# Optimization experiments

Hardware: AMD Instinct MI355X
Metric: run time of the kernel (lower is better)

## Reference

```python
import jax, jax.numpy as jnp
import numpy as np

N, E, G, D, L = 10000, 160000, 100, 128, 5
LMAX, SHD, VOCAB = 2, 9, 10
S3 = 3.0 ** 0.5


def _sph(v):
    # e3nn spherical harmonics, normalize=True, normalization='norm' (||Y_l||=1), lmax=2
    r = jnp.linalg.norm(v, axis=-1, keepdims=True)
    u = v / jnp.maximum(r, 1e-12)
    x, y, z = u[:, 0], u[:, 1], u[:, 2]
    y2 = jnp.stack([S3 * x * z, S3 * x * y, y * y - 0.5 * (x * x + z * z), S3 * y * z, 0.5 * S3 * (z * z - x * x)], axis=-1)
    return jnp.concatenate([jnp.ones_like(u[:, :1]), u, y2], axis=-1)  # [E,9]


def _sh_scale(s, w):
    # FullyConnectedTensorProduct(sh, 1x0e, sh): per-l scaling by weight w [.,3]
    return jnp.concatenate([s[:, 0:1] * w[:, 0:1], s[:, 1:4] * w[:, 1:2], s[:, 4:9] * w[:, 2:3]], axis=-1)


def _smean(src, idx, n):
    s = jax.ops.segment_sum(src, idx, num_segments=n)
    c = jax.ops.segment_sum(jnp.ones((src.shape[0], 1), src.dtype), idx, num_segments=n)
    return s / jnp.maximum(c, 1.0)


def _mlp(x, w1, b1, w2, b2, last_act=False):
    h = jax.nn.silu(x @ w1 + b1)
    o = h @ w2 + b2
    return jax.nn.silu(o) if last_act else o


def _forward(atoms, edge_index, batch_ids, pos, emb_table, Wsi1, bsi1, Wsi2, bsi2, WsiC1, bsiC1, WsiC2, bsiC2, Wm1, bm1, Wm2, bm2, Wp1, bp1, Wp2, bp2, Wn1, bn1, Wn2, bn2, Ws1, bs1, Ws2, bs2, Wpred, bpred):
    row, col = edge_index[0], edge_index[1]
    feat = emb_table[atoms]                                  # [N,D]
    # --- SH_INIT ---
    dpos = pos[row] - pos[col]
    dist = jnp.linalg.norm(dpos, axis=-1, keepdims=True)
    msg = _mlp(jnp.concatenate([dist, feat[row], feat[col]], axis=-1), Wsi1, bsi1, Wsi2, bsi2)
    dsh = _sh_scale(jax.lax.stop_gradient(_sph(dpos)), msg)
    sh = _smean(dsh, row, N)                                 # [N,9]
    pos_com = _smean(pos, batch_ids, G)[batch_ids]
    sh = sh + _sh_scale(jax.lax.stop_gradient(_sph(pos - pos_com)), _mlp(feat, WsiC1, bsiC1, WsiC2, bsiC2))
    sh = sh.at[:, :LMAX * LMAX].set(0.0)                     # all_ell=False: keep only highest l
    # --- stacked HEGNN layers via scan ---
    def body(carry, p):
        feat, pos, sh = carry
        wm1, cm1, wm2, cm2, wp1, cp1, wp2, cp2, wn1, cn1, wn2, cn2, ws1, cs1, ws2, cs2 = p
        dp = pos[row] - pos[col]
        d2 = jnp.sum(dp * dp, axis=-1, keepdims=True)        # squared distance
        t = sh[row] * sh[col]
        ip = jnp.concatenate([jnp.sum(t[:, 0:1], -1, keepdims=True), jnp.sum(t[:, 1:4], -1, keepdims=True), jnp.sum(t[:, 4:9], -1, keepdims=True)], axis=-1)
        m = _mlp(jnp.concatenate([feat[row], feat[col], d2, ip], axis=-1), wm1, cm1, wm2, cm2, last_act=True)
        dp = dp * _mlp(m, wp1, cp1, wp2, cp2)
        ds = _sh_scale(sh[row] - sh[col], _mlp(m, ws1, cs1, ws2, cs2))
        m_agg = _smean(m, row, N)
        p_agg = _smean(dp, row, N)
        s_agg = _smean(ds, row, N)
        sh = sh + s_agg
        pos = pos + p_agg
        feat = _mlp(jnp.concatenate([feat, m_agg], axis=-1), wn1, cn1, wn2, cn2)
        return (feat, pos, sh), None
    (feat, pos, sh), _ = jax.lax.scan(body, (feat, pos, sh), (Wm1, bm1, Wm2, bm2, Wp1, bp1, Wp2, bp2, Wn1, bn1, Wn2, bn2, Ws1, bs1, Ws2, bs2))
    # --- equivariant sum-pool + linear pred ---
    pooled = jax.ops.segment_sum(jnp.concatenate([feat, pos, sh], axis=-1), batch_ids, num_segments=G)
    return pooled @ Wpred + bpred                            # [G,1]


def setup_inputs():
    ks = iter(jax.random.split(jax.random.key(0), 48))
    def nrm(shape):
        return jax.random.normal(next(ks), shape, jnp.float32)
    def w(shape):
        return nrm(shape) / np.float32(np.sqrt(shape[-2]))
    z = lambda *s: jnp.zeros(s, jnp.float32)
    inp = dict(
        atoms=jax.random.randint(next(ks), (N,), 0, VOCAB),
        edge_index=jax.random.randint(next(ks), (2, E), 0, N),
        batch_ids=jnp.sort(jax.random.randint(next(ks), (N,), 0, G)),
        pos=nrm((N, 3)),
        emb_table=nrm((VOCAB, D)) * 0.1,
    )
    inp.update(Wsi1=w((2 * D + 1, D)), bsi1=z(D), Wsi2=w((D, LMAX + 1)), bsi2=z(LMAX + 1),
               WsiC1=w((D, D)), bsiC1=z(D), WsiC2=w((D, LMAX + 1)), bsiC2=z(LMAX + 1))
    inp.update(Wm1=w((L, 2 * D + 1 + LMAX + 1, D)), bm1=z(L, D), Wm2=w((L, D, D)), bm2=z(L, D),
               Wp1=w((L, D, D)), bp1=z(L, D), Wp2=w((L, D, 1)), bp2=z(L, 1),
               Wn1=w((L, 2 * D, D)), bn1=z(L, D), Wn2=w((L, D, D)), bn2=z(L, D),
               Ws1=w((L, D, D)), bs1=z(L, D), Ws2=w((L, D, LMAX + 1)), bs2=z(L, LMAX + 1),
               Wpred=w((D + 3 + SHD, 1)), bpred=z(1))
    return inp


def reference(atoms, edge_index, batch_ids, pos, emb_table, Wsi1, bsi1, Wsi2, bsi2, WsiC1, bsiC1, WsiC2, bsiC2, Wm1, bm1, Wm2, bm2, Wp1, bp1, Wp2, bp2, Wn1, bn1, Wn2, bn2, Ws1, bs1, Ws2, bs2, Wpred, bpred):
    return _forward(atoms, edge_index, batch_ids, pos, emb_table, Wsi1, bsi1, Wsi2, bsi2, WsiC1, bsiC1, WsiC2, bsiC2, Wm1, bm1, Wm2, bm2, Wp1, bp1, Wp2, bp2, Wn1, bn1, Wn2, bn2, Ws1, bs1, Ws2, bs2, Wpred, bpred)
```

## Files before the change

### kernel.cpp

```cpp
#include <hip/hip_runtime.h>
#include <math.h>

#define NA 10000
#define NE 160000
#define NG 100
#define DF 128
#define NL 5
#define NAP 10112
#define NSB 40

typedef __attribute__((ext_vector_type(8))) short bfx8;
typedef __attribute__((ext_vector_type(4))) float f32x4;

__device__ __forceinline__ float silu_f(float x) {
    return x / (1.0f + __expf(-x));
}

__device__ __forceinline__ unsigned short f2bf(float x) {
    unsigned u = __builtin_bit_cast(unsigned, x);
    u = (u + 0x7FFFu + ((u >> 16) & 1u)) >> 16;
    return (unsigned short)u;
}
__device__ __forceinline__ float bf2f(unsigned short h) {
    unsigned u = ((unsigned)h) << 16;
    return __builtin_bit_cast(float, u);
}
__device__ __forceinline__ unsigned packbf(float lo, float hi) {
    return (unsigned)f2bf(lo) | ((unsigned)f2bf(hi) << 16);
}

__device__ __forceinline__ void sph9(float dx, float dy, float dz, float* s) {
    float r = sqrtf(dx * dx + dy * dy + dz * dz);
    float inv = 1.0f / fmaxf(r, 1e-12f);
    float x = dx * inv, y = dy * inv, z = dz * inv;
    const float S3 = 1.7320508075688772f;
    s[0] = 1.0f;
    s[1] = x; s[2] = y; s[3] = z;
    s[4] = S3 * x * z;
    s[5] = S3 * x * y;
    s[6] = y * y - 0.5f * (x * x + z * z);
    s[7] = S3 * y * z;
    s[8] = 0.5f * S3 * (z * z - x * x);
}

#define OFF_SI1   0
#define OFF_SIC1  36864
#define LBASE     53248
#define LSIZE     135168
#define LOFF_M1   0
#define LOFF_M2   36864
#define LOFF_P1   53248
#define LOFF_S1   69632
#define LOFF_N1   86016
#define LOFF_N2   118784
#define WT_TOTAL  729088

__global__ void k_prep_w(const float* __restrict__ Wsi1, const float* __restrict__ WsiC1,
                         const float* __restrict__ Wm1, const float* __restrict__ Wm2,
                         const float* __restrict__ Wp1, const float* __restrict__ Ws1,
                         const float* __restrict__ Wn1, const float* __restrict__ Wn2,
                         unsigned short* __restrict__ WT) {
    int flat = blockIdx.x * 256 + threadIdx.x;
    if (flat >= WT_TOTAL) return;
    float v = 0.0f;
    if (flat < OFF_SIC1) {
        int o = flat - OFF_SI1;
        int n = o / 288, k = o % 288;
        if (k < 256)       v = Wsi1[(k + 1) * 128 + n];
        else if (k == 256) v = Wsi1[n];
    } else if (flat < LBASE) {
        int o = flat - OFF_SIC1;
        int n = o / 128, k = o % 128;
        v = WsiC1[k * 128 + n];
    } else {
        int t = flat - LBASE;
        int lyr = t / LSIZE;
        int o = t % LSIZE;
        if (o < LOFF_M2) {
            int n = o / 288, k = o % 288;
            if (k < 260) v = Wm1[(size_t)lyr * 260 * 128 + k * 128 + n];
        } else if (o < LOFF_P1) {
            int o2 = o - LOFF_M2; int n = o2 / 128, k = o2 % 128;
            v = Wm2[(size_t)lyr * 16384 + k * 128 + n];
        } else if (o < LOFF_S1) {
            int o2 = o - LOFF_P1; int n = o2 / 128, k = o2 % 128;
            v = Wp1[(size_t)lyr * 16384 + k * 128 + n];
        } else if (o < LOFF_N1) {
            int o2 = o - LOFF_S1; int n = o2 / 128, k = o2 % 128;
            v = Ws1[(size_t)lyr * 16384 + k * 128 + n];
        } else if (o < LOFF_N2) {
            int o2 = o - LOFF_N1; int n = o2 / 256, k = o2 % 256;
            v = Wn1[(size_t)lyr * 32768 + k * 128 + n];
        } else {
            int o2 = o - LOFF_N2; int n = o2 / 128, k = o2 % 128;
            v = Wn2[(size_t)lyr * 16384 + k * 128 + n];
        }
    }
    WT[flat] = f2bf(v);
}

template <int KP, int MODE, bool ACT, int NOUT, bool F32OUT>
__global__ __launch_bounds__(256) void gemm_mfma(
    const unsigned short* __restrict__ Ab,
    const unsigned short* __restrict__ WT,
    const float* __restrict__ bias, int M,
    const int* __restrict__ rowI, const int* __restrict__ colI,
    const unsigned short* __restrict__ featb, const unsigned short* __restrict__ tailb,
    unsigned short* __restrict__ Cb, float* __restrict__ Cf,
    const float* __restrict__ W2, const float* __restrict__ b2,
    float* __restrict__ outS)
{
    constexpr int NO = (NOUT > 0) ? NOUT : 1;
    __shared__ unsigned short As[128 * 40];
    __shared__ unsigned short Bs[128 * 40];
    __shared__ float W2s[NOUT > 0 ? 128 * NO : 1];
    __shared__ float red[NOUT > 0 ? 128 * 8 * NO : 1];

    const int tid = threadIdx.x;
    const int m0 = blockIdx.x * 128;
    const int mlo = tid >> 2;
    const int part = tid & 3;

    if (NOUT > 0) {
        for (int t = tid; t < 128 * NO; t += 256) W2s[t] = W2[t];
    }

    int er0 = 0, ec0 = 0, er1 = 0, ec1 = 0;
    if (MODE == 1) {
        er0 = rowI[m0 + mlo];      ec0 = colI[m0 + mlo];
        er1 = rowI[m0 + mlo + 64]; ec1 = colI[m0 + mlo + 64];
    }

    const int w = tid >> 6;
    const int l = tid & 63;
    const int quad = l >> 4;
    const int lm = l & 15;
    const int wm = (w >> 1) * 64, wn = (w & 1) * 64;

    float bv[4];
#pragma unroll
    for (int j = 0; j < 4; j++) bv[j] = bias[wn + j * 16 + lm];

    f32x4 acc[4][4] = {};

    constexpr int NCH = KP / 32;
#pragma unroll 1
    for (int c = 0; c < NCH; c++) {
        const int k0 = c * 32;
#pragma unroll
        for (int i = 0; i < 2; i++) {
            const int m = mlo + i * 64;
            uint4 v;
            if (MODE == 0) {
                v = *(const uint4*)(Ab + (size_t)(m0 + m) * KP + k0 + part * 8);
            } else {
                if (k0 < 128) {
                    int e = i ? er1 : er0;
                    v = *(const uint4*)(featb + (size_t)e * 128 + k0 + part * 8);
                } else if (k0 < 256) {
                    int e = i ? ec1 : ec0;
                    v = *(const uint4*)(featb + (size_t)e * 128 + (k0 - 128) + part * 8);
                } else {
                    if (part == 0) v = *(const uint4*)(tailb + (size_t)(m0 + m) * 16);
                    else           v = make_uint4(0, 0, 0, 0);
                }
            }
            *(uint4*)&As[m * 40 + part * 8] = v;
            uint4 wv = *(const uint4*)(WT + (size_t)m * KP + k0 + part * 8);
            *(uint4*)&Bs[m * 40 + part * 8] = wv;
        }
        __syncthreads();
        bfx8 a[4], b[4];
#pragma unroll
        for (int i = 0; i < 4; i++) a[i] = *(const bfx8*)&As[(wm + i * 16 + lm) * 40 + quad * 8];
#pragma unroll
        for (int j = 0; j < 4; j++) b[j] = *(const bfx8*)&Bs[(wn + j * 16 + lm) * 40 + quad * 8];
#pragma unroll
        for (int i = 0; i < 4; i++)
#pragma unroll
            for (int j = 0; j < 4; j++)
                acc[i][j] = __builtin_amdgcn_mfma_f32_16x16x32_bf16(a[i], b[j], acc[i][j], 0, 0, 0);
        __syncthreads();
    }

    if (NOUT > 0) {
        const int slot = (w & 1) * 4 + (lm >> 2);
#pragma unroll
        for (int i = 0; i < 4; i++) {
#pragma unroll
            for (int r = 0; r < 4; r++) {
                const int rowL = wm + i * 16 + quad * 4 + r;
                float ps[NO];
#pragma unroll
                for (int o = 0; o < NO; o++) ps[o] = 0.0f;
#pragma unroll
                for (int j = 0; j < 4; j++) {
                    float v = silu_f(acc[i][j][r] + bv[j]);
                    const int colg = wn + j * 16 + lm;
#pragma unroll
                    for (int o = 0; o < NO; o++) ps[o] += v * W2s[colg * NO + o];
                }
#pragma unroll
                for (int off = 1; off <= 2; off <<= 1)
#pragma unroll
                    for (int o = 0; o < NO; o++) ps[o] += __shfl_xor(ps[o], off, 64);
                if ((lm & 3) == 0)
#pragma unroll
                    for (int o = 0; o < NO; o++)
                        red[(rowL * 8 + slot) * NO + o] = ps[o];
            }
        }
        __syncthreads();
        for (int t = tid; t < 128 * NO; t += 256) {
            int rowL = t / NO, o = t - rowL * NO;
            float s = 0.0f;
#pragma unroll
            for (int k = 0; k < 8; k++) s += red[(rowL * 8 + k) * NO + o];
            int e = m0 + rowL;
            if (e < M) outS[(size_t)e * NO + o] = s + b2[o];
        }
    } else {
#pragma unroll
        for (int i = 0; i < 4; i++) {
            const int rbase = wm + i * 16 + quad * 4;
#pragma unroll
            for (int r = 0; r < 4; r++) {
                const int e = m0 + rbase + r;
                if (e >= M) continue;
#pragma unroll
                for (int j = 0; j < 4; j++) {
                    float v = acc[i][j][r] + bv[j];
                    if (ACT) v = silu_f(v);
                    const int colg = wn + j * 16 + lm;
                    Cb[(size_t)e * 128 + colg] = f2bf(v);
                    if (F32OUT) Cf[(size_t)e * 128 + colg] = v;
                }
            }
        }
    }
}

__global__ void k_count_edges(const int* __restrict__ row, int* __restrict__ cnt) {
    int e = blockIdx.x * blockDim.x + threadIdx.x;
    if (e < NE) atomicAdd(&cnt[row[e]], 1);
}

__global__ void k_scan_block(const int* __restrict__ cnt, int* __restrict__ ptr,
                             int* __restrict__ btot) {
    __shared__ int s[256];
    int tid = threadIdx.x;
    int i = blockIdx.x * 256 + tid;
    int v = (i < NA) ? cnt[i] : 0;
    s[tid] = v;
    __syncthreads();
    for (int off = 1; off < 256; off <<= 1) {
        int t = (tid >= off) ? s[tid - off] : 0;
        __syncthreads();
        s[tid] += t;
        __syncthreads();
    }
    if (i < NA) ptr[i] = s[tid] - v;
    if (tid == 255) btot[blockIdx.x] = s[255];
}

__global__ void k_scan_tot(int* __restrict__ btot) {
    int lane = threadIdx.x;
    int v = (lane < NSB) ? btot[lane] : 0;
    int orig = v;
    for (int off = 1; off < 64; off <<= 1) {
        int t = __shfl_up(v, off, 64);
        if (lane >= off) v += t;
    }
    if (lane < NSB) btot[lane] = v - orig;
}

__global__ void k_scan_add(int* __restrict__ ptr, const int* __restrict__ btot) {
    int i = blockIdx.x * 256 + threadIdx.x;
    if (i < NA) ptr[i] += btot[i >> 8];
    if (i == 0) ptr[NA] = NE;
}

__global__ void k_copy_cursor(const int* __restrict__ ptr, int* __restrict__ cursor) {
    int i = blockIdx.x * 256 + threadIdx.x;
    if (i < NA) cursor[i] = ptr[i];
}

__global__ void k_sort(const int* __restrict__ row, const int* __restrict__ col,
                       int* __restrict__ cursor,
                       int* __restrict__ row_s, int* __restrict__ col_s) {
    int e = blockIdx.x * blockDim.x + threadIdx.x;
    if (e >= NE) return;
    int r = row[e];
    int p = atomicAdd(&cursor[r], 1);
    row_s[p] = r;
    col_s[p] = col[e];
}

__global__ void k_gptr(const int* __restrict__ bid, int* __restrict__ gptr) {
    int n = blockIdx.x * blockDim.x + threadIdx.x;
    if (n >= NA) return;
    int b = bid[n];
    int bp = (n == 0) ? -1 : bid[n - 1];
    for (int g = bp + 1; g <= b; g++) gptr[g] = n;
    if (n == NA - 1)
        for (int g = b + 1; g <= NG; g++) gptr[g] = NA;
}

__global__ void k_init_feat(const int* __restrict__ atoms,
                            const float* __restrict__ emb,
                            float* __restrict__ feat, unsigned short* __restrict__ featb) {
    int idx = blockIdx.x * blockDim.x + threadIdx.x;
    if (idx >= NA * DF) return;
    float v = emb[atoms[idx >> 7] * DF + (idx & 127)];
    feat[idx] = v;
    featb[idx] = f2bf(v);
}

__global__ void k_copy_pos(const float* __restrict__ pos, float* __restrict__ posc) {
    int idx = blockIdx.x * blockDim.x + threadIdx.x;
    if (idx < NA * 3) posc[idx] = pos[idx];
}

__global__ void k_com_g(const float* __restrict__ pos, const int* __restrict__ gptr,
                        float* __restrict__ com) {
    int g = blockIdx.x;
    int lane = threadIdx.x;
    int s0 = gptr[g], s1 = gptr[g + 1];
    float sx = 0.0f, sy = 0.0f, sz = 0.0f;
    for (int n = s0 + lane; n < s1; n += 64) {
        sx += pos[n * 3 + 0];
        sy += pos[n * 3 + 1];
        sz += pos[n * 3 + 2];
    }
#pragma unroll
    for (int off = 32; off > 0; off >>= 1) {
        sx += __shfl_down(sx, off, 64);
        sy += __shfl_down(sy, off, 64);
        sz += __shfl_down(sz, off, 64);
    }
    if (lane == 0) {
        float cinv = 1.0f / fmaxf((float)(s1 - s0), 1.0f);
        com[g * 3 + 0] = sx * cinv;
        com[g * 3 + 1] = sy * cinv;
        com[g * 3 + 2] = sz * cinv;
    }
}

__global__ void k_tail_init(const int* __restrict__ row, const int* __restrict__ col,
                            const float* __restrict__ pos, unsigned short* __restrict__ tailb) {
    int e = blockIdx.x * blockDim.x + threadIdx.x;
    if (e >= NE) return;
    int r = row[e], c = col[e];
    float dx = pos[r * 3 + 0] - pos[c * 3 + 0];
    float dy = pos[r * 3 + 1] - pos[c * 3 + 1];
    float dz = pos[r * 3 + 2] - pos[c * 3 + 2];
    float dist = sqrtf(dx * dx + dy * dy + dz * dz);
    uint4 t0 = make_uint4(packbf(dist, 0.0f), 0, 0, 0);
    uint4 z = make_uint4(0, 0, 0, 0);
    *(uint4*)(tailb + (size_t)e * 16) = t0;
    *(uint4*)(tailb + (size_t)e * 16 + 8) = z;
}

__global__ void k_edge_pre(const int* __restrict__ row, const int* __restrict__ col,
                           const float* __restrict__ pos, const float* __restrict__ sh,
                           unsigned short* __restrict__ tailb) {
    int e = blockIdx.x * blockDim.x + threadIdx.x;
    if (e >= NE) return;
    int r = row[e], c = col[e];
    float dx = pos[r * 3 + 0] - pos[c * 3 + 0];
    float dy = pos[r * 3 + 1] - pos[c * 3 + 1];
    float dz = pos[r * 3 + 2] - pos[c * 3 + 2];
    float d2 = dx * dx + dy * dy + dz * dz;
    const float* sr = sh + (size_t)r * 9;
    const float* sc = sh + (size_t)c * 9;
    float ip0 = sr[0] * sc[0];
    float ip1 = sr[1] * sc[1] + sr[2] * sc[2] + sr[3] * sc[3];
    float ip2 = sr[4] * sc[4] + sr[5] * sc[5] + sr[6] * sc[6] + sr[7] * sc[7] + sr[8] * sc[8];
    uint4 t0 = make_uint4(packbf(d2, ip0), packbf(ip1, ip2), 0, 0);
    uint4 z = make_uint4(0, 0, 0, 0);
    *(uint4*)(tailb + (size_t)e * 16) = t0;
    *(uint4*)(tailb + (size_t)e * 16 + 8) = z;
}

__global__ void k_gather_sph(const int* __restrict__ ptr, const int* __restrict__ col_s,
                             const float* __restrict__ pos, const float* __restrict__ msg,
                             float* __restrict__ sh_mean) {
    int n = blockIdx.x;
    int lane = threadIdx.x;
    int s0 = ptr[n], s1 = ptr[n + 1];
    float px = pos[n * 3 + 0], py = pos[n * 3 + 1], pz = pos[n * 3 + 2];
    float a[9];
#pragma unroll
    for (int j = 0; j < 9; j++) a[j] = 0.0f;
    for (int e = s0 + lane; e < s1; e += 64) {
        int c = col_s[e];
        float dx = px - pos[c * 3 + 0];
        float dy = py - pos[c * 3 + 1];
        float dz = pz - pos[c * 3 + 2];
        float s[9];
        sph9(dx, dy, dz, s);
        float w0 = msg[e * 3 + 0], w1 = msg[e * 3 + 1], w2 = msg[e * 3 + 2];
        a[0] += s[0] * w0;
        a[1] += s[1] * w1; a[2] += s[2] * w1; a[3] += s[3] * w1;
        a[4] += s[4] * w2; a[5] += s[5] * w2; a[6] += s[6] * w2;
        a[7] += s[7] * w2; a[8] += s[8] * w2;
    }
#pragma unroll
    for (int off = 32; off > 0; off >>= 1)
#pragma unroll
        for (int j = 0; j < 9; j++) a[j] += __shfl_down(a[j], off, 64);
    if (lane == 0) {
        float cinv = 1.0f / fmaxf((float)(s1 - s0), 1.0f);
#pragma unroll
        for (int j = 0; j < 9; j++) sh_mean[(size_t)n * 9 + j] = a[j] * cinv;
    }
}

__global__ void k_sh_finish(const float* __restrict__ sh_mean,
                            const float* __restrict__ pos, const float* __restrict__ com,
                            const int* __restrict__ bid, const float* __restrict__ msgC,
                            float* __restrict__ sh) {
    int n = blockIdx.x * blockDim.x + threadIdx.x;
    if (n >= NA) return;
    int b = bid[n];
    float dx = pos[n * 3 + 0] - com[b * 3 + 0];
    float dy = pos[n * 3 + 1] - com[b * 3 + 1];
    float dz = pos[n * 3 + 2] - com[b * 3 + 2];
    float s[9];
    sph9(dx, dy, dz, s);
    float w2 = msgC[n * 3 + 2];
    sh[n * 9 + 0] = 0.0f;
    sh[n * 9 + 1] = 0.0f;
    sh[n * 9 + 2] = 0.0f;
    sh[n * 9 + 3] = 0.0f;
#pragma unroll
    for (int j = 4; j < 9; j++)
        sh[n * 9 + j] = sh_mean[(size_t)n * 9 + j] + s[j] * w2;
}

__global__ void k_gather_ps_upd(const int* __restrict__ ptr, const int* __restrict__ col_s,
                                const float* __restrict__ pos, const float* __restrict__ sh,
                                const float* __restrict__ psc, const float* __restrict__ ssc,
                                float* __restrict__ pos_new, float* __restrict__ sh_new) {
    int n = blockIdx.x;
    int lane = threadIdx.x;
    int s0 = ptr[n], s1 = ptr[n + 1];
    float px = pos[n * 3 + 0], py = pos[n * 3 + 1], pz = pos[n * 3 + 2];
    float shn[9];
#pragma unroll
    for (int j = 0; j < 9; j++) shn[j] = sh[(size_t)n * 9 + j];
    float a[12];
#pragma unroll
    for (int j = 0; j < 12; j++) a[j] = 0.0f;
    for (int e = s0 + lane; e < s1; e += 64) {
        int c = col_s[e];
        float p = psc[e];
        a[0] += (px - pos[c * 3 + 0]) * p;
        a[1] += (py - pos[c * 3 + 1]) * p;
        a[2] += (pz - pos[c * 3 + 2]) * p;
        float w0 = ssc[e * 3 + 0], w1 = ssc[e * 3 + 1], w2 = ssc[e * 3 + 2];
        const float* sc = sh + (size_t)c * 9;
        a[3]  += (shn[0] - sc[0]) * w0;
        a[4]  += (shn[1] - sc[1]) * w1;
        a[5]  += (shn[2] - sc[2]) * w1;
        a[6]  += (shn[3] - sc[3]) * w1;
        a[7]  += (shn[4] - sc[4]) * w2;
        a[8]  += (shn[5] - sc[5]) * w2;
        a[9]  += (shn[6] - sc[6]) * w2;
        a[10] += (shn[7] - sc[7]) * w2;
        a[11] += (shn[8] - sc[8]) * w2;
    }
#pragma unroll
    for (int off = 32; off > 0; off >>= 1)
#pragma unroll
        for (int j = 0; j < 12; j++) a[j] += __shfl_down(a[j], off, 64);
    if (lane == 0) {
        float cinv = 1.0f / fmaxf((float)(s1 - s0), 1.0f);
        pos_new[n * 3 + 0] = px + a[0] * cinv;
        pos_new[n * 3 + 1] = py + a[1] * cinv;
        pos_new[n * 3 + 2] = pz + a[2] * cinv;
#pragma unroll
        for (int j = 0; j < 9; j++) sh_new[(size_t)n * 9 + j] = shn[j] + a[3 + j] * cinv;
    }
}

__global__ __launch_bounds__(128) void k_gather_xn(
    const int* __restrict__ ptr, const unsigned short* __restrict__ bufMb,
    const unsigned short* __restrict__ featb, unsigned short* __restrict__ Xnb) {
    int n = blockIdx.x;
    int c = threadIdx.x;
    int s0 = ptr[n], s1 = ptr[n + 1];
    float sum = 0.0f;
    for (int e = s0; e < s1; e++) sum += bf2f(bufMb[(size_t)e * 128 + c]);
    float cinv = 1.0f / fmaxf((float)(s1 - s0), 1.0f);
    Xnb[(size_t)n * 256 + c] = featb[(size_t)n * 128 + c];
    Xnb[(size_t)n * 256 + 128 + c] = f2bf(sum * cinv);
}

__global__ __launch_bounds__(192) void k_pool_pred(
    const int* __restrict__ gptr, const float* __restrict__ feat,
    const float* __restrict__ pos, const float* __restrict__ sh,
    const float* __restrict__ Wp, const float* __restrict__ bp,
    float* __restrict__ out) {
    __shared__ float pl[140];
    int g = blockIdx.x;
    int c = threadIdx.x;
    int s0 = gptr[g], s1 = gptr[g + 1];
    if (c < 140) {
        float sum = 0.0f;
        for (int n = s0; n < s1; n++) {
            float v;
            if (c < 128)      v = feat[(size_t)n * 128 + c];
            else if (c < 131) v = pos[n * 3 + (c - 128)];
            else              v = sh[(size_t)n * 9 + (c - 131)];
            sum += v;
        }
        pl[c] = sum;
    }
    __syncthreads();
    if (c < 64) {
        float s = 0.0f;
        for (int k = c; k < 140; k += 64) s += pl[k] * Wp[k];
#pragma unroll
        for (int off = 32; off > 0; off >>= 1) s += __shfl_down(s, off, 64);
        if (c == 0) out[g] = s + bp[0];
    }
}

extern "C" void kernel_launch(void* const* d_in, const int* in_sizes, int n_in,
                              void* d_out, int out_size, void* d_ws, size_t ws_size,
                              hipStream_t stream) {
    const int*   atoms  = (const int*)d_in[0];
    const int*   eidx   = (const int*)d_in[1];
    const int*   row    = eidx;
    const int*   col    = eidx + NE;
    const int*   bid    = (const int*)d_in[2];
    const float* pos_in = (const float*)d_in[3];
    const float* emb    = (const float*)d_in[4];
    const float* Wsi1   = (const float*)d_in[5];
    const float* bsi1   = (const float*)d_in[6];
    const float* Wsi2   = (const float*)d_in[7];
    const float* bsi2   = (const float*)d_in[8];
    const float* WsiC1  = (const float*)d_in[9];
    const float* bsiC1  = (const float*)d_in[10];
    const float* WsiC2  = (const float*)d_in[11];
    const float* bsiC2  = (const float*)d_in[12];
    const float* Wm1    = (const float*)d_in[13];
    const float* bm1    = (const float*)d_in[14];
    const float* Wm2    = (const float*)d_in[15];
    const float* bm2    = (const float*)d_in[16];
    const float* Wp1    = (const float*)d_in[17];
    const float* bp1    = (const float*)d_in[18];
    const float* Wp2    = (const float*)d_in[19];
    const float* bp2    = (const float*)d_in[20];
    const float* Wn1    = (const float*)d_in[21];
    const float* bn1    = (const float*)d_in[22];
    const float* Wn2    = (const float*)d_in[23];
    const float* bn2    = (const float*)d_in[24];
    const float* Ws1    = (const float*)d_in[25];
    const float* bs1    = (const float*)d_in[26];
    const float* Ws2    = (const float*)d_in[27];
    const float* bs2    = (const float*)d_in[28];
    const float* Wpred  = (const float*)d_in[29];
    const float* bpred  = (const float*)d_in[30];

    float* base = (float*)d_ws;
    size_t off = 0;
    auto alloc = [&](size_t nfl) { float* r = base + off; off += nfl; return r; };
    unsigned short* bufHb = (unsigned short*)alloc((size_t)NE * DF / 2);
    unsigned short* bufMb = (unsigned short*)alloc((size_t)NE * DF / 2);
    unsigned short* featb = (unsigned short*)alloc((size_t)NAP * DF / 2);
    unsigned short* hnb   = (unsigned short*)alloc((size_t)NAP * DF / 2);
    unsigned short* Xnb   = (unsigned short*)alloc((size_t)NAP * 256 / 2);
    unsigned short* tailb = (unsigned short*)alloc((size_t)NE * 16 / 2);
    unsigned short* WT    = (unsigned short*)alloc(WT_TOTAL / 2);
    float* feat    = alloc((size_t)NAP * DF);
    float* sc3     = alloc((size_t)NE * 3);
    float* psc     = alloc(NE);
    float* pos0    = alloc((size_t)NA * 3 + 4);
    float* pos1    = alloc((size_t)NA * 3 + 4);
    float* sh0     = alloc((size_t)NA * 9 + 4);
    float* sh1     = alloc((size_t)NA * 9 + 4);
    float* sh_mean = alloc((size_t)NA * 9 + 4);
    float* com     = alloc(NG * 3 + 4);
    float* msgC    = alloc((size_t)NA * 3 + 4);
    int* cnt_row   = (int*)alloc(NA);
    int* ptr       = (int*)alloc(NA + 4);
    int* cursor    = (int*)alloc(NA);
    int* gptr      = (int*)alloc(NG + 4);
    int* row_s     = (int*)alloc(NE);
    int* col_s     = (int*)alloc(NE);
    int* btot      = (int*)alloc(64);

    const dim3 B256(256);
    const int gE = NE / 128;
    const int gN = NAP / 128;

    hipMemsetAsync(cnt_row, 0, NA * sizeof(int), stream);
    k_prep_w<<<(WT_TOTAL + 255) / 256, B256, 0, stream>>>(Wsi1, WsiC1, Wm1, Wm2, Wp1, Ws1, Wn1, Wn2, WT);
    k_init_feat<<<(NA * DF + 255) / 256, B256, 0, stream>>>(atoms, emb, feat, featb);
    k_copy_pos<<<(NA * 3 + 255) / 256, B256, 0, stream>>>(pos_in, pos0);
    k_count_edges<<<(NE + 255) / 256, B256, 0, stream>>>(row, cnt_row);
    k_scan_block<<<NSB, B256, 0, stream>>>(cnt_row, ptr, btot);
    k_scan_tot<<<1, 64, 0, stream>>>(btot);
    k_scan_add<<<NSB, B256, 0, stream>>>(ptr, btot);
    k_copy_cursor<<<NSB, B256, 0, stream>>>(ptr, cursor);
    k_sort<<<(NE + 255) / 256, B256, 0, stream>>>(row, col, cursor, row_s, col_s);
    k_gptr<<<(NA + 255) / 256, B256, 0, stream>>>(bid, gptr);
    k_com_g<<<NG, 64, 0, stream>>>(pos_in, gptr, com);

    k_tail_init<<<(NE + 255) / 256, B256, 0, stream>>>(row_s, col_s, pos0, tailb);
    gemm_mfma<288, 1, true, 3, false><<<gE, B256, 0, stream>>>(
        nullptr, WT + OFF_SI1, bsi1, NE, row_s, col_s, featb, tailb,
        nullptr, nullptr, Wsi2, bsi2, sc3);
    k_gather_sph<<<NA, 64, 0, stream>>>(ptr, col_s, pos0, sc3, sh_mean);
    gemm_mfma<128, 0, true, 3, false><<<gN, B256, 0, stream>>>(
        featb, WT + OFF_SIC1, bsiC1, NA, nullptr, nullptr, nullptr, nullptr,
        nullptr, nullptr, WsiC2, bsiC2, msgC);
    k_sh_finish<<<(NA + 255) / 256, B256, 0, stream>>>(sh_mean, pos0, com, bid, msgC, sh0);

    float* posA = pos0; float* posB = pos1;
    float* shA = sh0;   float* shB = sh1;

    for (int l = 0; l < NL; l++) {
        const unsigned short* wtL = WT + LBASE + (size_t)l * LSIZE;
        const float* cm1 = bm1 + l * 128;
        const float* cm2 = bm2 + l * 128;
        const float* cp1 = bp1 + l * 128;
        const float* wp2 = Wp2 + (size_t)l * 128;
        const float* cp2 = bp2 + l;
        const float* cn1 = bn1 + l * 128;
        const float* cn2 = bn2 + l * 128;
        const float* cs1 = bs1 + l * 128;
        const float* ws2 = Ws2 + (size_t)l * 128 * 3;
        const float* cs2 = bs2 + l * 3;

        k_edge_pre<<<(NE + 255) / 256, B256, 0, stream>>>(row_s, col_s, posA, shA, tailb);
        gemm_mfma<288, 1, true, 0, false><<<gE, B256, 0, stream>>>(
            nullptr, wtL + LOFF_M1, cm1, NE, row_s, col_s, featb, tailb,
            bufHb, nullptr, nullptr, nullptr, nullptr);
        gemm_mfma<128, 0, true, 0, false><<<gE, B256, 0, stream>>>(
            bufHb, wtL + LOFF_M2, cm2, NE, nullptr, nullptr, nullptr, nullptr,
            bufMb, nullptr, nullptr, nullptr, nullptr);
        gemm_mfma<128, 0, true, 1, false><<<gE, B256, 0, stream>>>(
            bufMb, wtL + LOFF_P1, cp1, NE, nullptr, nullptr, nullptr, nullptr,
            nullptr, nullptr, wp2, cp2, psc);
        gemm_mfma<128, 0, true, 3, false><<<gE, B256, 0, stream>>>(
            bufMb, wtL + LOFF_S1, cs1, NE, nullptr, nullptr, nullptr, nullptr,
            nullptr, nullptr, ws2, cs2, sc3);
        k_gather_ps_upd<<<NA, 64, 0, stream>>>(ptr, col_s, posA, shA, psc, sc3, posB, shB);
        k_gather_xn<<<NA, 128, 0, stream>>>(ptr, bufMb, featb, Xnb);
        gemm_mfma<256, 0, true, 0, false><<<gN, B256, 0, stream>>>(
            Xnb, wtL + LOFF_N1, cn1, NA, nullptr, nullptr, nullptr, nullptr,
            hnb, nullptr, nullptr, nullptr, nullptr);
        gemm_mfma<128, 0, false, 0, true><<<gN, B256, 0, stream>>>(
            hnb, wtL + LOFF_N2, cn2, NA, nullptr, nullptr, nullptr, nullptr,
            featb, feat, nullptr, nullptr, nullptr);

        float* tp = posA; posA = posB; posB = tp;
        float* ts = shA;  shA = shB;  shB = ts;
    }

    k_pool_pred<<<NG, 192, 0, stream>>>(gptr, feat, posA, shA, Wpred, bpred, (float*)d_out);
}
```

Before: 1.046 ms.

## Factor edge first-layer GEMM into per-node projections plus edge gather-add

The first edge MLP layer on concat(feat[row], feat[col], scalars) is split algebraically. feat@W_row and feat@W_col are computed once per node (10k rows) with a new dual GEMM. Each edge then gathers the two projected rows, adds the scalar-tail terms and bias in fp32, and applies SiLU, which removes a K=288 GEMM over 160k edges in the init and every layer. The position/SH gather kernel is also merged with the feature-mean gather to save a launch. The per-node projections are rounded to bf16 before summation, which slightly changes numerics.

```diff
diff --git a/kernel.cpp b/kernel.cpp
--- a/kernel.cpp
+++ b/kernel.cpp
@@ -43,17 +43,17 @@
     s[8] = 0.5f * S3 * (z * z - x * x);
 }
 
-#define OFF_SI1   0
-#define OFF_SIC1  36864
-#define LBASE     53248
-#define LSIZE     135168
-#define LOFF_M1   0
-#define LOFF_M2   36864
-#define LOFF_P1   53248
-#define LOFF_S1   69632
-#define LOFF_N1   86016
-#define LOFF_N2   118784
-#define WT_TOTAL  729088
+#define OFF_SIRC  0
+#define OFF_SICTR 32768
+#define LBASE     49152
+#define LOFF_MRC  0
+#define LOFF_M2   32768
+#define LOFF_P1   49152
+#define LOFF_S1   65536
+#define LOFF_N1   81920
+#define LOFF_N2   114688
+#define LSIZE     131072
+#define WT_TOTAL  704512
 
 __global__ void k_prep_w(const float* __restrict__ Wsi1, const float* __restrict__ WsiC1,
                          const float* __restrict__ Wm1, const float* __restrict__ Wm2,
@@ -63,49 +63,105 @@
     int flat = blockIdx.x * 256 + threadIdx.x;
     if (flat >= WT_TOTAL) return;
     float v = 0.0f;
-    if (flat < OFF_SIC1) {
-        int o = flat - OFF_SI1;
-        int n = o / 288, k = o % 288;
-        if (k < 256)       v = Wsi1[(k + 1) * 128 + n];
-        else if (k == 256) v = Wsi1[n];
+    if (flat < OFF_SICTR) {
+        int half = flat >> 14;
+        int o = flat & 16383;
+        int n = o >> 7, k = o & 127;
+        v = Wsi1[(k + 1 + half * 128) * 128 + n];
     } else if (flat < LBASE) {
-        int o = flat - OFF_SIC1;
-        int n = o / 128, k = o % 128;
+        int o = flat - OFF_SICTR;
+        int n = o >> 7, k = o & 127;
         v = WsiC1[k * 128 + n];
     } else {
         int t = flat - LBASE;
         int lyr = t / LSIZE;
         int o = t % LSIZE;
         if (o < LOFF_M2) {
-            int n = o / 288, k = o % 288;
-            if (k < 260) v = Wm1[(size_t)lyr * 260 * 128 + k * 128 + n];
+            int half = o >> 14;
+            int o2 = o & 16383;
+            int n = o2 >> 7, k = o2 & 127;
+            v = Wm1[(size_t)lyr * 33280 + (k + half * 128) * 128 + n];
         } else if (o < LOFF_P1) {
-            int o2 = o - LOFF_M2; int n = o2 / 128, k = o2 % 128;
+            int o2 = o - LOFF_M2; int n = o2 >> 7, k = o2 & 127;
             v = Wm2[(size_t)lyr * 16384 + k * 128 + n];
         } else if (o < LOFF_S1) {
-            int o2 = o - LOFF_P1; int n = o2 / 128, k = o2 % 128;
+            int o2 = o - LOFF_P1; int n = o2 >> 7, k = o2 & 127;
             v = Wp1[(size_t)lyr * 16384 + k * 128 + n];
         } else if (o < LOFF_N1) {
-            int o2 = o - LOFF_S1; int n = o2 / 128, k = o2 % 128;
+            int o2 = o - LOFF_S1; int n = o2 >> 7, k = o2 & 127;
             v = Ws1[(size_t)lyr * 16384 + k * 128 + n];
         } else if (o < LOFF_N2) {
-            int o2 = o - LOFF_N1; int n = o2 / 256, k = o2 % 256;
+            int o2 = o - LOFF_N1; int n = o2 >> 8, k = o2 & 255;
             v = Wn1[(size_t)lyr * 32768 + k * 128 + n];
         } else {
-            int o2 = o - LOFF_N2; int n = o2 / 128, k = o2 % 128;
+            int o2 = o - LOFF_N2; int n = o2 >> 7, k = o2 & 127;
             v = Wn2[(size_t)lyr * 16384 + k * 128 + n];
         }
     }
     WT[flat] = f2bf(v);
 }
 
-template <int KP, int MODE, bool ACT, int NOUT, bool F32OUT>
+__global__ __launch_bounds__(256) void k_fgemm(
+    const unsigned short* __restrict__ Ab,
+    const unsigned short* __restrict__ WT2,
+    unsigned short* __restrict__ F12)
+{
+    __shared__ unsigned short As[128 * 40];
+    __shared__ unsigned short Bs[128 * 40];
+    const unsigned short* WTp = WT2 + (size_t)blockIdx.y * 16384;
+    unsigned short* Cb = F12 + (size_t)blockIdx.y * NAP * 128;
+
+    const int tid = threadIdx.x;
+    const int m0 = blockIdx.x * 128;
+    const int mlo = tid >> 2;
+    const int part = tid & 3;
+    const int w = tid >> 6, l = tid & 63;
+    const int quad = l >> 4, lm = l & 15;
+    const int wm = (w >> 1) * 64, wn = (w & 1) * 64;
+
+    f32x4 acc[4][4] = {};
+#pragma unroll 1
+    for (int c = 0; c < 4; c++) {
+        const int k0 = c * 32;
+#pragma unroll
+        for (int i = 0; i < 2; i++) {
+            const int m = mlo + i * 64;
+            *(uint4*)&As[m * 40 + part * 8] =
+                *(const uint4*)(Ab + (size_t)(m0 + m) * 128 + k0 + part * 8);
+            *(uint4*)&Bs[m * 40 + part * 8] =
+                *(const uint4*)(WTp + (size_t)m * 128 + k0 + part * 8);
+        }
+        __syncthreads();
+        bfx8 a[4], b[4];
+#pragma unroll
+        for (int i = 0; i < 4; i++) a[i] = *(const bfx8*)&As[(wm + i * 16 + lm) * 40 + quad * 8];
+#pragma unroll
+        for (int j = 0; j < 4; j++) b[j] = *(const bfx8*)&Bs[(wn + j * 16 + lm) * 40 + quad * 8];
+#pragma unroll
+        for (int i = 0; i < 4; i++)
+#pragma unroll
+            for (int j = 0; j < 4; j++)
+                acc[i][j] = __builtin_amdgcn_mfma_f32_16x16x32_bf16(a[i], b[j], acc[i][j], 0, 0, 0);
+        __syncthreads();
+    }
+#pragma unroll
+    for (int i = 0; i < 4; i++) {
+        const int rbase = wm + i * 16 + quad * 4;
+#pragma unroll
+        for (int r = 0; r < 4; r++) {
+            const int e = m0 + rbase + r;
+#pragma unroll
+            for (int j = 0; j < 4; j++)
+                Cb[(size_t)e * 128 + wn + j * 16 + lm] = f2bf(acc[i][j][r]);
+        }
+    }
+}
+
+template <int KP, bool ACT, int NOUT, bool F32OUT>
 __global__ __launch_bounds__(256) void gemm_mfma(
     const unsigned short* __restrict__ Ab,
     const unsigned short* __restrict__ WT,
     const float* __restrict__ bias, int M,
-    const int* __restrict__ rowI, const int* __restrict__ colI,
-    const unsigned short* __restrict__ featb, const unsigned short* __restrict__ tailb,
     unsigned short* __restrict__ Cb, float* __restrict__ Cf,
     const float* __restrict__ W2, const float* __restrict__ b2,
     float* __restrict__ outS)
@@ -125,16 +181,8 @@
         for (int t = tid; t < 128 * NO; t += 256) W2s[t] = W2[t];
     }
 
-    int er0 = 0, ec0 = 0, er1 = 0, ec1 = 0;
-    if (MODE == 1) {
-        er0 = rowI[m0 + mlo];      ec0 = colI[m0 + mlo];
-        er1 = rowI[m0 + mlo + 64]; ec1 = colI[m0 + mlo + 64];
-    }
-
-    const int w = tid >> 6;
-    const int l = tid & 63;
-    const int quad = l >> 4;
-    const int lm = l & 15;
+    const int w = tid >> 6, l = tid & 63;
+    const int quad = l >> 4, lm = l & 15;
     const int wm = (w >> 1) * 64, wn = (w & 1) * 64;
 
     float bv[4];
@@ -142,7 +190,6 @@
     for (int j = 0; j < 4; j++) bv[j] = bias[wn + j * 16 + lm];
 
     f32x4 acc[4][4] = {};
-
     constexpr int NCH = KP / 32;
 #pragma unroll 1
     for (int c = 0; c < NCH; c++) {
@@ -150,24 +197,10 @@
 #pragma unroll
         for (int i = 0; i < 2; i++) {
             const int m = mlo + i * 64;
-            uint4 v;
-            if (MODE == 0) {
-                v = *(const uint4*)(Ab + (size_t)(m0 + m) * KP + k0 + part * 8);
-            } else {
-                if (k0 < 128) {
-                    int e = i ? er1 : er0;
-                    v = *(const uint4*)(featb + (size_t)e * 128 + k0 + part * 8);
-                } else if (k0 < 256) {
-                    int e = i ? ec1 : ec0;
-                    v = *(const uint4*)(featb + (size_t)e * 128 + (k0 - 128) + part * 8);
-                } else {
-                    if (part == 0) v = *(const uint4*)(tailb + (size_t)(m0 + m) * 16);
-                    else           v = make_uint4(0, 0, 0, 0);
-                }
-            }
-            *(uint4*)&As[m * 40 + part * 8] = v;
-            uint4 wv = *(const uint4*)(WT + (size_t)m * KP + k0 + part * 8);
-            *(uint4*)&Bs[m * 40 + part * 8] = wv;
+            *(uint4*)&As[m * 40 + part * 8] =
+                *(const uint4*)(Ab + (size_t)(m0 + m) * KP + k0 + part * 8);
+            *(uint4*)&Bs[m * 40 + part * 8] =
+                *(const uint4*)(WT + (size_t)m * KP + k0 + part * 8);
         }
         __syncthreads();
         bfx8 a[4], b[4];
@@ -237,6 +270,120 @@
                 }
             }
         }
+    }
+}
+
+__global__ __launch_bounds__(256) void k_edge_h(
+    const int* __restrict__ rowI, const int* __restrict__ colI,
+    const unsigned short* __restrict__ F12,
+    const float* __restrict__ pos, const float* __restrict__ sh,
+    const float* __restrict__ wtail,
+    const float* __restrict__ b1,
+    unsigned short* __restrict__ bufHb)
+{
+    __shared__ float Wt[4][128];
+    __shared__ float B1[128];
+    int tid = threadIdx.x;
+    if (tid < 128) B1[tid] = b1[tid];
+    for (int t = tid; t < 512; t += 256) Wt[t >> 7][t & 127] = wtail[t];
+    __syncthreads();
+
+    int eloc = tid >> 1;
+    int half = tid & 1;
+    int e = blockIdx.x * 128 + eloc;
+    int r = rowI[e], c = colI[e];
+
+    float dx = pos[r * 3 + 0] - pos[c * 3 + 0];
+    float dy = pos[r * 3 + 1] - pos[c * 3 + 1];
+    float dz = pos[r * 3 + 2] - pos[c * 3 + 2];
+    float d2 = dx * dx + dy * dy + dz * dz;
+    const float* sr = sh + (size_t)r * 9;
+    const float* sc = sh + (size_t)c * 9;
+    float ip0 = sr[0] * sc[0];
+    float ip1 = sr[1] * sc[1] + sr[2] * sc[2] + sr[3] * sc[3];
+    float ip2 = sr[4] * sc[4] + sr[5] * sc[5] + sr[6] * sc[6] + sr[7] * sc[7] + sr[8] * sc[8];
+
+    const unsigned short* f1 = F12 + (size_t)r * 128 + half * 64;
+    const unsigned short* f2 = F12 + (size_t)NAP * 128 + (size_t)c * 128 + half * 64;
+    unsigned short* outp = bufHb + (size_t)e * 128 + half * 64;
+    const int jb = half * 64;
+
+#pragma unroll
+    for (int blk = 0; blk < 8; blk++) {
+        uint4 a = *(const uint4*)(f1 + blk * 8);
+        uint4 b = *(const uint4*)(f2 + blk * 8);
+        unsigned av[4] = {a.x, a.y, a.z, a.w};
+        unsigned bvv[4] = {b.x, b.y, b.z, b.w};
+        unsigned ov[4];
+#pragma unroll
+        for (int q = 0; q < 4; q++) {
+            int j0 = jb + blk * 8 + q * 2;
+            float h0 = bf2f((unsigned short)(av[q] & 0xFFFFu)) + bf2f((unsigned short)(bvv[q] & 0xFFFFu))
+                     + d2 * Wt[0][j0] + ip0 * Wt[1][j0] + ip1 * Wt[2][j0] + ip2 * Wt[3][j0] + B1[j0];
+            float h1 = bf2f((unsigned short)(av[q] >> 16)) + bf2f((unsigned short)(bvv[q] >> 16))
+                     + d2 * Wt[0][j0 + 1] + ip0 * Wt[1][j0 + 1] + ip1 * Wt[2][j0 + 1] + ip2 * Wt[3][j0 + 1] + B1[j0 + 1];
+            ov[q] = packbf(silu_f(h0), silu_f(h1));
+        }
+        *(uint4*)(outp + blk * 8) = make_uint4(ov[0], ov[1], ov[2], ov[3]);
+    }
+}
+
+__global__ __launch_bounds__(256) void k_edge_si(
+    const int* __restrict__ rowI, const int* __restrict__ colI,
+    const unsigned short* __restrict__ F12,
+    const float* __restrict__ pos,
+    const float* __restrict__ Wsi1,
+    const float* __restrict__ b1,
+    const float* __restrict__ W2,
+    const float* __restrict__ b2,
+    float* __restrict__ outS)
+{
+    __shared__ float Wd[128];
+    __shared__ float B1[128];
+    __shared__ float W2s[128 * 3];
+    int tid = threadIdx.x;
+    if (tid < 128) { Wd[tid] = Wsi1[tid]; B1[tid] = b1[tid]; }
+    for (int t = tid; t < 384; t += 256) W2s[t] = W2[t];
+    __syncthreads();
+
+    int eloc = tid >> 1;
+    int half = tid & 1;
+    int e = blockIdx.x * 128 + eloc;
+    int r = rowI[e], c = colI[e];
+
+    float dx = pos[r * 3 + 0] - pos[c * 3 + 0];
+    float dy = pos[r * 3 + 1] - pos[c * 3 + 1];
+    float dz = pos[r * 3 + 2] - pos[c * 3 + 2];
+    float dist = sqrtf(dx * dx + dy * dy + dz * dz);
+
+    const unsigned short* f1 = F12 + (size_t)r * 128 + half * 64;
+    const unsigned short* f2 = F12 + (size_t)NAP * 128 + (size_t)c * 128 + half * 64;
+    const int jb = half * 64;
+
+    float ps[3] = {0.0f, 0.0f, 0.0f};
+#pragma unroll
+    for (int blk = 0; blk < 8; blk++) {
+        uint4 a = *(const uint4*)(f1 + blk * 8);
+        uint4 b = *(const uint4*)(f2 + blk * 8);
+        unsigned av[4] = {a.x, a.y, a.z, a.w};
+        unsigned bvv[4] = {b.x, b.y, b.z, b.w};
+#pragma unroll
+        for (int q = 0; q < 4; q++) {
+            int j0 = jb + blk * 8 + q * 2;
+            float h0 = silu_f(bf2f((unsigned short)(av[q] & 0xFFFFu)) + bf2f((unsigned short)(bvv[q] & 0xFFFFu))
+                              + dist * Wd[j0] + B1[j0]);
+            float h1 = silu_f(bf2f((unsigned short)(av[q] >> 16)) + bf2f((unsigned short)(bvv[q] >> 16))
+                              + dist * Wd[j0 + 1] + B1[j0 + 1]);
+#pragma unroll
+            for (int o = 0; o < 3; o++)
+                ps[o] += h0 * W2s[j0 * 3 + o] + h1 * W2s[(j0 + 1) * 3 + o];
+        }
+    }
+#pragma unroll
+    for (int o = 0; o < 3; o++) ps[o] += __shfl_xor(ps[o], 1, 64);
+    if (half == 0) {
+#pragma unroll
+        for (int o = 0; o < 3; o++) outS[(size_t)e * 3 + o] = ps[o] + b2[o];
     }
 }
 
@@ -344,42 +491,6 @@
         com[g * 3 + 1] = sy * cinv;
         com[g * 3 + 2] = sz * cinv;
     }
-}
-
-__global__ void k_tail_init(const int* __restrict__ row, const int* __restrict__ col,
-                            const float* __restrict__ pos, unsigned short* __restrict__ tailb) {
-    int e = blockIdx.x * blockDim.x + threadIdx.x;
-    if (e >= NE) return;
-    int r = row[e], c = col[e];
-    float dx = pos[r * 3 + 0] - pos[c * 3 + 0];
-    float dy = pos[r * 3 + 1] - pos[c * 3 + 1];
-    float dz = pos[r * 3 + 2] - pos[c * 3 + 2];
-    float dist = sqrtf(dx * dx + dy * dy + dz * dz);
-    uint4 t0 = make_uint4(packbf(dist, 0.0f), 0, 0, 0);
-    uint4 z = make_uint4(0, 0, 0, 0);
-    *(uint4*)(tailb + (size_t)e * 16) = t0;
-    *(uint4*)(tailb + (size_t)e * 16 + 8) = z;
-}
-
-__global__ void k_edge_pre(const int* __restrict__ row, const int* __restrict__ col,
-                           const float* __restrict__ pos, const float* __restrict__ sh,
-                           unsigned short* __restrict__ tailb) {
-    int e = blockIdx.x * blockDim.x + threadIdx.x;
-    if (e >= NE) return;
-    int r = row[e], c = col[e];
-    float dx = pos[r * 3 + 0] - pos[c * 3 + 0];
-    float dy = pos[r * 3 + 1] - pos[c * 3 + 1];
-    float dz = pos[r * 3 + 2] - pos[c * 3 + 2];
-    float d2 = dx * dx + dy * dy + dz * dz;
-    const float* sr = sh + (size_t)r * 9;
-    const float* sc = sh + (size_t)c * 9;
-    float ip0 = sr[0] * sc[0];
-    float ip1 = sr[1] * sc[1] + sr[2] * sc[2] + sr[3] * sc[3];
-    float ip2 = sr[4] * sc[4] + sr[5] * sc[5] + sr[6] * sc[6] + sr[7] * sc[7] + sr[8] * sc[8];
-    uint4 t0 = make_uint4(packbf(d2, ip0), packbf(ip1, ip2), 0, 0);
-    uint4 z = make_uint4(0, 0, 0, 0);
-    *(uint4*)(tailb + (size_t)e * 16) = t0;
-    *(uint4*)(tailb + (size_t)e * 16 + 8) = z;
 }
 
 __global__ void k_gather_sph(const int* __restrict__ ptr, const int* __restrict__ col_s,
@@ -438,63 +549,63 @@
         sh[n * 9 + j] = sh_mean[(size_t)n * 9 + j] + s[j] * w2;
 }
 
-__global__ void k_gather_ps_upd(const int* __restrict__ ptr, const int* __restrict__ col_s,
-                                const float* __restrict__ pos, const float* __restrict__ sh,
-                                const float* __restrict__ psc, const float* __restrict__ ssc,
-                                float* __restrict__ pos_new, float* __restrict__ sh_new) {
+__global__ __launch_bounds__(128) void k_gather_nx(
+    const int* __restrict__ ptr, const int* __restrict__ col_s,
+    const unsigned short* __restrict__ bufMb, const unsigned short* __restrict__ featb,
+    const float* __restrict__ pos, const float* __restrict__ sh,
+    const float* __restrict__ psc, const float* __restrict__ ssc,
+    unsigned short* __restrict__ Xnb,
+    float* __restrict__ pos_new, float* __restrict__ sh_new)
+{
     int n = blockIdx.x;
-    int lane = threadIdx.x;
+    int tid = threadIdx.x;
     int s0 = ptr[n], s1 = ptr[n + 1];
-    float px = pos[n * 3 + 0], py = pos[n * 3 + 1], pz = pos[n * 3 + 2];
-    float shn[9];
-#pragma unroll
-    for (int j = 0; j < 9; j++) shn[j] = sh[(size_t)n * 9 + j];
-    float a[12];
-#pragma unroll
-    for (int j = 0; j < 12; j++) a[j] = 0.0f;
-    for (int e = s0 + lane; e < s1; e += 64) {
-        int c = col_s[e];
-        float p = psc[e];
-        a[0] += (px - pos[c * 3 + 0]) * p;
-        a[1] += (py - pos[c * 3 + 1]) * p;
-        a[2] += (pz - pos[c * 3 + 2]) * p;
-        float w0 = ssc[e * 3 + 0], w1 = ssc[e * 3 + 1], w2 = ssc[e * 3 + 2];
-        const float* sc = sh + (size_t)c * 9;
-        a[3]  += (shn[0] - sc[0]) * w0;
-        a[4]  += (shn[1] - sc[1]) * w1;
-        a[5]  += (shn[2] - sc[2]) * w1;
-        a[6]  += (shn[3] - sc[3]) * w1;
-        a[7]  += (shn[4] - sc[4]) * w2;
-        a[8]  += (shn[5] - sc[5]) * w2;
-        a[9]  += (shn[6] - sc[6]) * w2;
-        a[10] += (shn[7] - sc[7]) * w2;
-        a[11] += (shn[8] - sc[8]) * w2;
-    }
-#pragma unroll
-    for (int off = 32; off > 0; off >>= 1)
-#pragma unroll
-        for (int j = 0; j < 12; j++) a[j] += __shfl_down(a[j], off, 64);
-    if (lane == 0) {
-        float cinv = 1.0f / fmaxf((float)(s1 - s0), 1.0f);
-        pos_new[n * 3 + 0] = px + a[0] * cinv;
-        pos_new[n * 3 + 1] = py + a[1] * cinv;
-        pos_new[n * 3 + 2] = pz + a[2] * cinv;
-#pragma unroll
-        for (int j = 0; j < 9; j++) sh_new[(size_t)n * 9 + j] = shn[j] + a[3 + j] * cinv;
-    }
-}
-
-__global__ __launch_bounds__(128) void k_gather_xn(
-    const int* __restrict__ ptr, const unsigned short* __restrict__ bufMb,
-    const unsigned short* __restrict__ featb, unsigned short* __restrict__ Xnb) {
-    int n = blockIdx.x;
-    int c = threadIdx.x;
-    int s0 = ptr[n], s1 = ptr[n + 1];
+    float cinv = 1.0f / fmaxf((float)(s1 - s0), 1.0f);
+
     float sum = 0.0f;
-    for (int e = s0; e < s1; e++) sum += bf2f(bufMb[(size_t)e * 128 + c]);
-    float cinv = 1.0f / fmaxf((float)(s1 - s0), 1.0f);
-    Xnb[(size_t)n * 256 + c] = featb[(size_t)n * 128 + c];
-    Xnb[(size_t)n * 256 + 128 + c] = f2bf(sum * cinv);
+    for (int e = s0; e < s1; e++) sum += bf2f(bufMb[(size_t)e * 128 + tid]);
+    Xnb[(size_t)n * 256 + tid] = featb[(size_t)n * 128 + tid];
+    Xnb[(size_t)n * 256 + 128 + tid] = f2bf(sum * cinv);
+
+    if (tid < 64) {
+        int lane = tid;
+        float px = pos[n * 3 + 0], py = pos[n * 3 + 1], pz = pos[n * 3 + 2];
+        float shn[9];
+#pragma unroll
+        for (int j = 0; j < 9; j++) shn[j] = sh[(size_t)n * 9 + j];
+        float a[12];
+#pragma unroll
+        for (int j = 0; j < 12; j++) a[j] = 0.0f;
+        for (int e = s0 + lane; e < s1; e += 64) {
+            int c = col_s[e];
+            float p = psc[e];
+            a[0] += (px - pos[c * 3 + 0]) * p;
+            a[1] += (py - pos[c * 3 + 1]) * p;
+            a[2] += (pz - pos[c * 3 + 2]) * p;
+            float w0 = ssc[e * 3 + 0], w1 = ssc[e * 3 + 1], w2 = ssc[e * 3 + 2];
+            const float* sc = sh + (size_t)c * 9;
+            a[3]  += (shn[0] - sc[0]) * w0;
+            a[4]  += (shn[1] - sc[1]) * w1;
+            a[5]  += (shn[2] - sc[2]) * w1;
+            a[6]  += (shn[3] - sc[3]) * w1;
+            a[7]  += (shn[4] - sc[4]) * w2;
+            a[8]  += (shn[5] - sc[5]) * w2;
+            a[9]  += (shn[6] - sc[6]) * w2;
+            a[10] += (shn[7] - sc[7]) * w2;
+            a[11] += (shn[8] - sc[8]) * w2;
+        }
+#pragma unroll
+        for (int off = 32; off > 0; off >>= 1)
+#pragma unroll
+            for (int j = 0; j < 12; j++) a[j] += __shfl_down(a[j], off, 64);
+        if (lane == 0) {
+            pos_new[n * 3 + 0] = px + a[0] * cinv;
+            pos_new[n * 3 + 1] = py + a[1] * cinv;
+            pos_new[n * 3 + 2] = pz + a[2] * cinv;
+#pragma unroll
+            for (int j = 0; j < 9; j++) sh_new[(size_t)n * 9 + j] = shn[j] + a[3 + j] * cinv;
+        }
+    }
 }
 
 __global__ __launch_bounds__(192) void k_pool_pred(
@@ -572,7 +683,7 @@
     unsigned short* featb = (unsigned short*)alloc((size_t)NAP * DF / 2);
     unsigned short* hnb   = (unsigned short*)alloc((size_t)NAP * DF / 2);
     unsigned short* Xnb   = (unsigned short*)alloc((size_t)NAP * 256 / 2);
-    unsigned short* tailb = (unsigned short*)alloc((size_t)NE * 16 / 2);
+    unsigned short* F12   = (unsigned short*)alloc((size_t)NAP * 256 / 2);
     unsigned short* WT    = (unsigned short*)alloc(WT_TOTAL / 2);
     float* feat    = alloc((size_t)NAP * DF);
     float* sc3     = alloc((size_t)NE * 3);
@@ -595,6 +706,7 @@
     const dim3 B256(256);
     const int gE = NE / 128;
     const int gN = NAP / 128;
+    const dim3 gF(gN, 2);
 
     hipMemsetAsync(cnt_row, 0, NA * sizeof(int), stream);
     k_prep_w<<<(WT_TOTAL + 255) / 256, B256, 0, stream>>>(Wsi1, WsiC1, Wm1, Wm2, Wp1, Ws1, Wn1, Wn2, WT);
@@ -609,14 +721,11 @@
     k_gptr<<<(NA + 255) / 256, B256, 0, stream>>>(bid, gptr);
     k_com_g<<<NG, 64, 0, stream>>>(pos_in, gptr, com);
 
-    k_tail_init<<<(NE + 255) / 256, B256, 0, stream>>>(row_s, col_s, pos0, tailb);
-    gemm_mfma<288, 1, true, 3, false><<<gE, B256, 0, stream>>>(
-        nullptr, WT + OFF_SI1, bsi1, NE, row_s, col_s, featb, tailb,
-        nullptr, nullptr, Wsi2, bsi2, sc3);
+    k_fgemm<<<gF, B256, 0, stream>>>(featb, WT + OFF_SIRC, F12);
+    k_edge_si<<<gE, B256, 0, stream>>>(row_s, col_s, F12, pos0, Wsi1, bsi1, Wsi2, bsi2, sc3);
     k_gather_sph<<<NA, 64, 0, stream>>>(ptr, col_s, pos0, sc3, sh_mean);
-    gemm_mfma<128, 0, true, 3, false><<<gN, B256, 0, stream>>>(
-        featb, WT + OFF_SIC1, bsiC1, NA, nullptr, nullptr, nullptr, nullptr,
-        nullptr, nullptr, WsiC2, bsiC2, msgC);
+    gemm_mfma<128, true, 3, false><<<gN, B256, 0, stream>>>(
+        featb, WT + OFF_SICTR, bsiC1, NA, nullptr, nullptr, WsiC2, bsiC2, msgC);
     k_sh_finish<<<(NA + 255) / 256, B256, 0, stream>>>(sh_mean, pos0, com, bid, msgC, sh0);
 
     float* posA = pos0; float* posB = pos1;
@@ -625,6 +734,7 @@
     for (int l = 0; l < NL; l++) {
         const unsigned short* wtL = WT + LBASE + (size_t)l * LSIZE;
         const float* cm1 = bm1 + l * 128;
+        const float* wtail = Wm1 + (size_t)l * 33280 + 256 * 128;
         const float* cm2 = bm2 + l * 128;
         const float* cp1 = bp1 + l * 128;
         const float* wp2 = Wp2 + (size_t)l * 128;
@@ -635,27 +745,20 @@
         const float* ws2 = Ws2 + (size_t)l * 128 * 3;
         const float* cs2 = bs2 + l * 3;
 
-        k_edge_pre<<<(NE + 255) / 256, B256, 0, stream>>>(row_s, col_s, posA, shA, tailb);
-        gemm_mfma<288, 1, true, 0, false><<<gE, B256, 0, stream>>>(
-            nullptr, wtL + LOFF_M1, cm1, NE, row_s, col_s, featb, tailb,
-            bufHb, nullptr, nullptr, nullptr, nullptr);
-        gemm_mfma<128, 0, true, 0, false><<<gE, B256, 0, stream>>>(
-            bufHb, wtL + LOFF_M2, cm2, NE, nullptr, nullptr, nullptr, nullptr,
-            bufMb, nullptr, nullptr, nullptr, nullptr);
-        gemm_mfma<128, 0, true, 1, false><<<gE, B256, 0, stream>>>(
-            bufMb, wtL + LOFF_P1, cp1, NE, nullptr, nullptr, nullptr, nullptr,
-            nullptr, nullptr, wp2, cp2, psc);
-        gemm_mfma<128, 0, true, 3, false><<<gE, B256, 0, stream>>>(
-            bufMb, wtL + LOFF_S1, cs1, NE, nullptr, nullptr, nullptr, nullptr,
-            nullptr, nullptr, ws2, cs2, sc3);
-        k_gather_ps_upd<<<NA, 64, 0, stream>>>(ptr, col_s, posA, shA, psc, sc3, posB, shB);
-        k_gather_xn<<<NA, 128, 0, stream>>>(ptr, bufMb, featb, Xnb);
-        gemm_mfma<256, 0, true, 0, false><<<gN, B256, 0, stream>>>(
-            Xnb, wtL + LOFF_N1, cn1, NA, nullptr, nullptr, nullptr, nullptr,
-            hnb, nullptr, nullptr, nullptr, nullptr);
-        gemm_mfma<128, 0, false, 0, true><<<gN, B256, 0, stream>>>(
-            hnb, wtL + LOFF_N2, cn2, NA, nullptr, nullptr, nullptr, nullptr,
-            featb, feat, nullptr, nullptr, nullptr);
+        k_fgemm<<<gF, B256, 0, stream>>>(featb, wtL + LOFF_MRC, F12);
+        k_edge_h<<<gE, B256, 0, stream>>>(row_s, col_s, F12, posA, shA, wtail, cm1, bufHb);
+        gemm_mfma<128, true, 0, false><<<gE, B256, 0, stream>>>(
+            bufHb, wtL + LOFF_M2, cm2, NE, bufMb, nullptr, nullptr, nullptr, nullptr);
+        gemm_mfma<128, true, 1, false><<<gE, B256, 0, stream>>>(
+            bufMb, wtL + LOFF_P1, cp1, NE, nullptr, nullptr, wp2, cp2, psc);
+        gemm_mfma<128, true, 3, false><<<gE, B256, 0, stream>>>(
+            bufMb, wtL + LOFF_S1, cs1, NE, nullptr, nullptr, ws2, cs2, sc3);
+        k_gather_nx<<<NA, 128, 0, stream>>>(ptr, col_s, bufMb, featb, posA, shA, psc, sc3,
+                                            Xnb, posB, shB);
+        gemm_mfma<256, true, 0, false><<<gN, B256, 0, stream>>>(
+            Xnb, wtL + LOFF_N1, cn1, NA, hnb, nullptr, nullptr, nullptr, nullptr);
+        gemm_mfma<128, false, 0, true><<<gN, B256, 0, stream>>>(
+            hnb, wtL + LOFF_N2, cn2, NA, featb, feat, nullptr, nullptr, nullptr);
 
         float* tp = posA; posA = posB; posB = tp;
         float* ts = shA;  shA = shB;  shB = ts;
```

Result: no change. 1.042 ms (-0.4%).
